# Kernel tuning notes

Hardware: AMD Instinct MI355X
Metric: run time of the kernel (lower is better)

## Reference

```python
import jax, jax.numpy as jnp
import numpy as np

ANCHORS = np.array([[10,13],[16,30],[33,23],[30,61],[62,45],[59,119],[116,90],[156,198],[373,326]], dtype=np.float32)
ANCHOR_MASK = [[6,7,8],[3,4,5],[0,1,2]]
CLASS_NUM = 80
IGNORE_THRESH = 0.5


def _bce_mean(z, x):
    # Keras BinaryCrossentropy(from_logits=True) called as a loss object:
    # elementwise sigmoid-CE, mean over last axis, then SUM_OVER_BATCH_SIZE
    # reduction == mean over ALL elements -> scalar.
    ce = jnp.maximum(x, 0.0) - x * z + jnp.log1p(jnp.exp(-jnp.abs(x)))
    return jnp.mean(ce)


def _layer_loss(out, lab, anchors):
    B, gh, gw, _ = out.shape
    A = anchors.shape[0]
    feats = out.reshape(B, gh, gw, A, CLASS_NUM + 5)
    anchors = jnp.asarray(anchors, dtype=jnp.float32)  # [A,2] (w,h)
    inp_wh = jnp.array([gw * 32, gh * 32], dtype=jnp.float32)  # reverse(input_shape)
    grid_wh = jnp.array([gw, gh], dtype=jnp.float32)           # reverse(grid_shape)

    gy, gx = jnp.meshgrid(jnp.arange(gh), jnp.arange(gw), indexing='ij')
    grid = jnp.stack([gx, gy], axis=-1).astype(jnp.float32)[:, :, None, :]  # [gh,gw,1,2]

    pred_xy = (jax.nn.sigmoid(feats[..., 0:2]) + grid) / grid_wh
    pred_wh = jnp.exp(feats[..., 2:4]) * anchors / inp_wh
    pred_box = jnp.concatenate([pred_xy, pred_wh], axis=-1)  # [B,gh,gw,A,4]

    obj = lab[..., 4:5]          # [B,gh,gw,A,1]
    objb = obj != 0.0
    N = gh * gw * A

    def _per_image(args):
        pb, tb, valid = args  # pb: [N,4] predicted, tb: [N,4] label boxes, valid: [N] bool
        b1_xy, b1_wh = pb[:, None, 0:2], pb[:, None, 2:4]
        b2_xy, b2_wh = tb[None, :, 0:2], tb[None, :, 2:4]
        b1_mins, b1_maxes = b1_xy - b1_wh / 2.0, b1_xy + b1_wh / 2.0
        b2_mins, b2_maxes = b2_xy - b2_wh / 2.0, b2_xy + b2_wh / 2.0
        inter_mins = jnp.maximum(b1_mins, b2_mins)
        inter_maxes = jnp.maximum(b1_maxes, b2_maxes)  # faithful to source (uses maximum, not minimum)
        inter_wh = jnp.maximum(inter_maxes - inter_mins, 0.0)
        inter = inter_wh[..., 0] * inter_wh[..., 1]
        a1 = b1_wh[..., 0] * b1_wh[..., 1]
        a2 = b2_wh[..., 0] * b2_wh[..., 1]
        iou = inter / (a1 + a2 - inter)  # [N,N]
        # only true boxes count; empty set -> best=-1 (matches tf reduce_max of empty = -inf)
        iou = jnp.where(valid[None, :], iou, -1.0)
        best_iou = jnp.max(iou, axis=-1)
        return (best_iou < IGNORE_THRESH).astype(jnp.float32)

    ignore = jax.lax.map(_per_image, (pred_box.reshape(B, N, 4),
                                      lab[..., 0:4].reshape(B, N, 4),
                                      objb.reshape(B, N)))
    ignore = jax.lax.stop_gradient(ignore).reshape(B, gh, gw, A, 1)

    raw_true_xy = lab[..., 0:2] * grid_wh - grid
    raw_true_wh = jnp.log(lab[..., 2:4] * inp_wh / anchors)
    raw_true_wh = jnp.where(objb, raw_true_wh, 0.0)
    box_loss_scale = 2.0 - lab[..., 2:3] * lab[..., 3:4]

    bf = jnp.float32(B)
    xy_loss = jnp.sum(obj * box_loss_scale * _bce_mean(raw_true_xy, feats[..., 0:2])) / bf
    wh_loss = jnp.sum(obj * box_loss_scale * 0.5 * jnp.square(raw_true_wh - feats[..., 2:4])) / bf
    conf_bce = _bce_mean(obj, feats[..., 4:5])
    conf_loss = jnp.sum(obj * conf_bce + (1.0 - obj) * conf_bce * ignore) / bf
    class_loss = jnp.sum(obj * _bce_mean(lab[..., 5:], feats[..., 5:])) / bf
    return xy_loss + wh_loss + conf_loss + class_loss


def _make_labels(key, B, g):
    k1, k2, k3, k4 = jax.random.split(key, 4)
    xy = jax.random.uniform(k1, (B, g, g, 3, 2), dtype=jnp.float32)
    wh = jax.random.uniform(k2, (B, g, g, 3, 2), dtype=jnp.float32, minval=0.05, maxval=1.0)
    objness = (jax.random.uniform(k3, (B, g, g, 3, 1)) < 0.02).astype(jnp.float32)
    cls = (jax.random.uniform(k4, (B, g, g, 3, CLASS_NUM)) < 0.05).astype(jnp.float32)
    return jnp.concatenate([xy, wh, objness, cls], axis=-1)


def setup_inputs() -> dict:
    key = jax.random.key(0)
    ks = jax.random.split(key, 6)
    B = 8
    grids = [13, 26, 52]
    out = {}
    for i, g in enumerate(grids):
        out[f'o{i}'] = jax.random.normal(ks[i], (B, g, g, 3 * (CLASS_NUM + 5)), dtype=jnp.float32)
        out[f'l{i}'] = _make_labels(ks[3 + i], B, g)
    return out


def reference(o0, o1, o2, l0, l1, l2):
    outputs = (o0, o1, o2)
    labels = (l0, l1, l2)
    loss = jnp.float32(0.0)
    for l in range(3):
        loss = loss + _layer_loss(outputs[l], labels[l], ANCHORS[ANCHOR_MASK[l]])
    return loss
```

## Files before the change

### kernel.cpp

```cpp
#include <hip/hip_runtime.h>
#include <math.h>

#define BDIM 256
#define NSTREAMB 1769
#define NCELLB 334
#define NBLK_A (NSTREAMB + NCELLB)

__device__ __constant__ float c_aw[3][3] = {{116.f,156.f,373.f},{30.f,62.f,59.f},{10.f,16.f,33.f}};
__device__ __constant__ float c_ah[3][3] = {{90.f,198.f,326.f},{61.f,45.f,119.f},{13.f,30.f,23.f}};


__device__ __forceinline__ float bce_fast(float z, float x) {
    float t = __expf(-fabsf(x));
    return fmaxf(x, 0.f) - x * z + __logf(1.f + t);
}
__device__ __forceinline__ float bce4(const float4& z, const float4& x) {
    return bce_fast(z.x, x.x) + bce_fast(z.y, x.y)
         + bce_fast(z.z, x.z) + bce_fast(z.w, x.w);
}

__global__ __launch_bounds__(BDIM) void mega_a(
    const float* __restrict__ o0, const float* __restrict__ l0,
    const float* __restrict__ o1, const float* __restrict__ l1,
    const float* __restrict__ o2, const float* __restrict__ l2,
    double* __restrict__ acc, int* __restrict__ cnt, float4* __restrict__ tbox,
    float4* __restrict__ pbox, float* __restrict__ noobj)
{
    if (blockIdx.x < NSTREAMB) {
        int layer, blk0, n4;
        const float4 *O4, *L4;
        if (blockIdx.x < 85)       { layer=0; blk0=0;   n4=86190;   O4=(const float4*)o0; L4=(const float4*)l0; }
        else if (blockIdx.x < 422) { layer=1; blk0=85;  n4=344760;  O4=(const float4*)o1; L4=(const float4*)l1; }
        else                       { layer=2; blk0=422; n4=1379040; O4=(const float4*)o2; L4=(const float4*)l2; }

        int rb   = (int)blockIdx.x - blk0;
        int base = rb * (BDIM * 4) + (int)threadIdx.x;
        float s0 = 0.f, s1 = 0.f, s2 = 0.f, s3 = 0.f;
        if ((rb + 1) * (BDIM * 4) <= n4) {
            float4 a0 = O4[base];          float4 b0 = L4[base];
            float4 a1 = O4[base +   BDIM]; float4 b1 = L4[base +   BDIM];
            float4 a2 = O4[base + 2*BDIM]; float4 b2 = L4[base + 2*BDIM];
            float4 a3 = O4[base + 3*BDIM]; float4 b3 = L4[base + 3*BDIM];
            s0 = bce4(b0, a0); s1 = bce4(b1, a1);
            s2 = bce4(b2, a2); s3 = bce4(b3, a3);
        } else {
            #pragma unroll
            for (int k = 0; k < 4; k++) {
                int j = base + k * BDIM;
                if (j < n4) { float4 a = O4[j], b = L4[j]; s0 += bce4(b, a); }
            }
        }
        float s = (s0 + s1) + (s2 + s3);
        __shared__ float sb[4];
        #pragma unroll
        for (int off = 32; off > 0; off >>= 1) s += __shfl_down(s, off, 64);
        if ((threadIdx.x & 63) == 0) sb[threadIdx.x >> 6] = s;
        __syncthreads();
        if (threadIdx.x == 0) {
            double t = (double)sb[0] + (double)sb[1] + (double)sb[2] + (double)sb[3];
            atomicAdd(&acc[layer * 8 + 0], t);
        }
        return;
    }

    int cb = blockIdx.x - NSTREAMB;
    int layer, blk0;
    if (cb < 16)      { layer = 0; blk0 = 0; }
    else if (cb < 80) { layer = 1; blk0 = 16; }
    else              { layer = 2; blk0 = 80; }
    const int g     = (layer == 0) ? 13 : (layer == 1) ? 26 : 52;
    const int Nlimg = g * g * 3;
    const int Cl    = 8 * Nlimg;
    const int cbase = (layer == 0) ? 0 : (layer == 1) ? 4056 : 20280;
    const float* O  = (layer == 0) ? o0 : (layer == 1) ? o1 : o2;
    const float* L  = (layer == 0) ? l0 : (layer == 1) ? l1 : l2;
    const float gf  = (float)g;
    const float inp = gf * 32.f;

    int cell = (cb - blk0) * BDIM + (int)threadIdx.x;
    float s_sub=0.f, s_xy=0.f, s_wh=0.f, s_conf=0.f, s_obj=0.f, s_s1=0.f;
    if (cell < Cl) {
        const float* op = O + (size_t)cell * 85;
        const float* lp = L + (size_t)cell * 85;
        float x0=op[0], x1=op[1], x2=op[2], x3=op[3], x4=op[4];
        float lx=lp[0], ly=lp[1], lw=lp[2], lh=lp[3], lobj=lp[4];
        int a  = cell % 3;
        int xi = (cell / 3) % g;
        int yi = (cell / (3 * g)) % g;
        int b  = cell / Nlimg;
        float aw = c_aw[layer][a], ah = c_ah[layer][a];

        float c4 = bce_fast(lobj, x4);
        s_sub  = bce_fast(lx,x0) + bce_fast(ly,x1)
               + bce_fast(lw,x2) + bce_fast(lh,x3) + c4;
        s_conf = c4;
        s_obj  = lobj;
        s_xy   = bce_fast(lx*gf - (float)xi, x0) + bce_fast(ly*gf - (float)yi, x1);

        float px = (1.f/(1.f+expf(-x0)) + (float)xi) / gf;
        float py = (1.f/(1.f+expf(-x1)) + (float)yi) / gf;
        float pw = expf(x2) * aw / inp;
        float ph = expf(x3) * ah / inp;
        pbox[cbase + cell]  = make_float4(px, py, pw, ph);
        noobj[cbase + cell] = 1.f - lobj;

        if (lobj != 0.f) {
            float bls = 2.f - lw * lh;
            s_s1 = lobj * bls;
            float dw = logf(lw * inp / aw) - x2;
            float dh = logf(lh * inp / ah) - x3;
            s_wh = lobj * bls * 0.5f * (dw * dw + dh * dh);
            int idx = atomicAdd(&cnt[layer * 8 + b], 1);
            tbox[cbase + b * Nlimg + idx] = make_float4(lx, ly, lw, lh);
        }
    }

    __shared__ float sb6[6][4];
    float v[6] = {s_sub, s_xy, s_wh, s_conf, s_obj, s_s1};
    #pragma unroll
    for (int q = 0; q < 6; q++) {
        float x = v[q];
        #pragma unroll
        for (int off = 32; off > 0; off >>= 1) x += __shfl_down(x, off, 64);
        if ((threadIdx.x & 63) == 0) sb6[q][threadIdx.x >> 6] = x;
    }
    __syncthreads();
    if (threadIdx.x < 6) {
        int q = threadIdx.x;
        double t = (double)sb6[q][0] + (double)sb6[q][1]
                 + (double)sb6[q][2] + (double)sb6[q][3];
        atomicAdd(&acc[layer * 8 + 1 + q], t);
    }
}

#define TCAP 512
#define NB_IGNORE 336
__global__ __launch_bounds__(BDIM) void ignore_fin(
    double* __restrict__ acc, const int* __restrict__ cnt,
    const float4* __restrict__ tbox, const float4* __restrict__ pbox,
    const float* __restrict__ noobj, int* __restrict__ done,
    float* __restrict__ out)
{
    int layer, img, chunk;
    if (blockIdx.x < 16)      { layer = 0; img = blockIdx.x >> 1; chunk = blockIdx.x & 1; }
    else if (blockIdx.x < 80) { int t = blockIdx.x - 16; layer = 1; img = t >> 3; chunk = t & 7; }
    else                      { int t = blockIdx.x - 80; layer = 2; img = t >> 5; chunk = t & 31; }
    const int g     = (layer == 0) ? 13 : (layer == 1) ? 26 : 52;
    const int Nlimg = g * g * 3;
    const int cbase = (layer == 0) ? 0 : (layer == 1) ? 4056 : 20280;

    int ci = chunk * BDIM + (int)threadIdx.x;
    bool live = (ci < Nlimg);
    int cell = cbase + img * Nlimg + (live ? ci : 0);

    float pminx=0, pmaxx=0, pminy=0, pmaxy=0, a1=0, nb=0;
    if (live) {
        float4 p = pbox[cell];
        pminx = p.x - p.z*0.5f; pmaxx = p.x + p.z*0.5f;
        pminy = p.y - p.w*0.5f; pmaxy = p.y + p.w*0.5f;
        a1 = p.z * p.w;
        nb = noobj[cell];
    }
    int n = cnt[layer * 8 + img];
    const float4* tp = tbox + cbase + img * Nlimg;

    __shared__ float4 sT[TCAP];
    float best = -1.f;
    bool donef = !live;
    for (int t0 = 0; t0 < n; t0 += TCAP) {
        int tn = min(TCAP, n - t0);
        __syncthreads();
        for (int i = threadIdx.x; i < tn; i += BDIM) sT[i] = tp[t0 + i];
        __syncthreads();
        if (!donef) {
            for (int j = 0; j < tn; j++) {
                float4 t = sT[j];
                float hw = t.z*0.5f, hh = t.w*0.5f;
                float imnx = fmaxf(pminx, t.x - hw);
                float imxx = fmaxf(pmaxx, t.x + hw);
                float imny = fmaxf(pminy, t.y - hh);
                float imxy = fmaxf(pmaxy, t.y + hh);
                float iw = fmaxf(imxx - imnx, 0.f);
                float ih = fmaxf(imxy - imny, 0.f);
                float inter = iw * ih;
                float iou = inter / (a1 + t.z*t.w - inter);
                best = fmaxf(best, iou);
                if (best >= 0.5f) { donef = true; break; }
            }
        }
    }
    float v = (live && best < 0.5f) ? nb : 0.f;

    __shared__ float sb[4];
    #pragma unroll
    for (int off = 32; off > 0; off >>= 1) v += __shfl_down(v, off, 64);
    if ((threadIdx.x & 63) == 0) sb[threadIdx.x >> 6] = v;
    __syncthreads();
    if (threadIdx.x == 0) {
        double t = (double)sb[0] + (double)sb[1] + (double)sb[2] + (double)sb[3];
        atomicAdd(&acc[layer * 8 + 7], t);
        __threadfence();
        int old = atomicAdd(done, 1);
        if (old == NB_IGNORE - 1) {
            __threadfence();
            double loss = 0.0;
            const int gs[3] = {13, 26, 52};
            for (int l = 0; l < 3; l++) {
                double C = 8.0 * gs[l] * gs[l] * 3.0;
                double q[8];
                #pragma unroll
                for (int k = 0; k < 8; k++)
                    q[k] = __hip_atomic_load(&acc[l*8+k], __ATOMIC_RELAXED,
                                             __HIP_MEMORY_SCOPE_AGENT);
                double cls = (q[0] - q[1]) / (C * 80.0);
                loss += ( (q[2]/(C*2.0))*q[6] + q[3]
                        + (q[4]/C)*(q[5]+q[7]) + cls*q[5] ) / 8.0;
            }
            out[0] = (float)loss;
        }
    }
}

extern "C" void kernel_launch(void* const* d_in, const int* in_sizes, int n_in,
                              void* d_out, int out_size, void* d_ws, size_t ws_size,
                              hipStream_t stream)
{
    const float* o0 = (const float*)d_in[0];
    const float* l0 = (const float*)d_in[1];
    const float* o1 = (const float*)d_in[2];
    const float* l1 = (const float*)d_in[3];
    const float* o2 = (const float*)d_in[4];
    const float* l2 = (const float*)d_in[5];

    double* acc   = (double*)d_ws;
    int*    cnt   = (int*)((char*)d_ws + 192);
    int*    done  = (int*)((char*)d_ws + 288);
    float4* tbox  = (float4*)((char*)d_ws + 512);
    float4* pbox  = (float4*)((char*)d_ws + 1363328);
    float*  noobj = (float*)((char*)d_ws + 2726144);

    hipMemsetAsync(d_ws, 0, 512, stream);
    mega_a<<<NBLK_A, BDIM, 0, stream>>>(o0, l0, o1, l1, o2, l2,
                                        acc, cnt, tbox, pbox, noobj);
    ignore_fin<<<NB_IGNORE, BDIM, 0, stream>>>(acc, cnt, tbox, pbox, noobj,
                                               done, (float*)d_out);
}
```

Measured before the change: 147.3 us.

## Replace global atomics with per-block slots and ballot compaction, drop memset

The first kernel stops issuing double atomics into shared accumulators and instead writes one partial sum per block into slot arrays. Label boxes are compacted within each block using a wavefront ballot and popcount, and stored with a per-block count, which replaces the per-image atomic counters. The ignore kernel now gathers the boxes for its image from the relevant block ranges, and the last block reduces all slots in parallel. Accumulators are zeroed inside the kernel, so the separate memset launch is gone. This removes atomic contention and one launch, at the cost of more gather and compaction work in the ignore kernel.

```diff
diff --git a/kernel.cpp b/kernel.cpp
--- a/kernel.cpp
+++ b/kernel.cpp
@@ -5,6 +5,8 @@
 #define NSTREAMB 1769
 #define NCELLB 334
 #define NBLK_A (NSTREAMB + NCELLB)
+#define NB_IGNORE 336
+#define TCAP 512
 
 __device__ __constant__ float c_aw[3][3] = {{116.f,156.f,373.f},{30.f,62.f,59.f},{10.f,16.f,33.f}};
 __device__ __constant__ float c_ah[3][3] = {{90.f,198.f,326.f},{61.f,45.f,119.f},{13.f,30.f,23.f}};
@@ -23,15 +25,21 @@
     const float* __restrict__ o0, const float* __restrict__ l0,
     const float* __restrict__ o1, const float* __restrict__ l1,
     const float* __restrict__ o2, const float* __restrict__ l2,
-    double* __restrict__ acc, int* __restrict__ cnt, float4* __restrict__ tbox,
-    float4* __restrict__ pbox, float* __restrict__ noobj)
+    double* __restrict__ accq7, int* __restrict__ done,
+    double* __restrict__ slotS, double* __restrict__ slotC,
+    int* __restrict__ countB, int* __restrict__ cidxB,
+    float4* __restrict__ tboxB, float4* __restrict__ pbox,
+    float* __restrict__ noobj)
 {
     if (blockIdx.x < NSTREAMB) {
-        int layer, blk0, n4;
+        if (blockIdx.x == 0 && threadIdx.x == 0) {
+            accq7[0] = 0.0; accq7[1] = 0.0; accq7[2] = 0.0; *done = 0;
+        }
+        int blk0, n4;
         const float4 *O4, *L4;
-        if (blockIdx.x < 85)       { layer=0; blk0=0;   n4=86190;   O4=(const float4*)o0; L4=(const float4*)l0; }
-        else if (blockIdx.x < 422) { layer=1; blk0=85;  n4=344760;  O4=(const float4*)o1; L4=(const float4*)l1; }
-        else                       { layer=2; blk0=422; n4=1379040; O4=(const float4*)o2; L4=(const float4*)l2; }
+        if (blockIdx.x < 85)       { blk0=0;   n4=86190;   O4=(const float4*)o0; L4=(const float4*)l0; }
+        else if (blockIdx.x < 422) { blk0=85;  n4=344760;  O4=(const float4*)o1; L4=(const float4*)l1; }
+        else                       { blk0=422; n4=1379040; O4=(const float4*)o2; L4=(const float4*)l2; }
 
         int rb   = (int)blockIdx.x - blk0;
         int base = rb * (BDIM * 4) + (int)threadIdx.x;
@@ -56,18 +64,17 @@
         for (int off = 32; off > 0; off >>= 1) s += __shfl_down(s, off, 64);
         if ((threadIdx.x & 63) == 0) sb[threadIdx.x >> 6] = s;
         __syncthreads();
-        if (threadIdx.x == 0) {
-            double t = (double)sb[0] + (double)sb[1] + (double)sb[2] + (double)sb[3];
-            atomicAdd(&acc[layer * 8 + 0], t);
-        }
+        if (threadIdx.x == 0)
+            slotS[blockIdx.x] = (double)sb[0] + (double)sb[1]
+                              + (double)sb[2] + (double)sb[3];
         return;
     }
 
     int cb = blockIdx.x - NSTREAMB;
-    int layer, blk0;
-    if (cb < 16)      { layer = 0; blk0 = 0; }
-    else if (cb < 80) { layer = 1; blk0 = 16; }
-    else              { layer = 2; blk0 = 80; }
+    int layer, cblk0;
+    if (cb < 16)      { layer = 0; cblk0 = 0; }
+    else if (cb < 80) { layer = 1; cblk0 = 16; }
+    else              { layer = 2; cblk0 = 80; }
     const int g     = (layer == 0) ? 13 : (layer == 1) ? 26 : 52;
     const int Nlimg = g * g * 3;
     const int Cl    = 8 * Nlimg;
@@ -77,9 +84,12 @@
     const float gf  = (float)g;
     const float inp = gf * 32.f;
 
-    int cell = (cb - blk0) * BDIM + (int)threadIdx.x;
+    int  cell = (cb - cblk0) * BDIM + (int)threadIdx.x;
+    bool live = (cell < Cl);
     float s_sub=0.f, s_xy=0.f, s_wh=0.f, s_conf=0.f, s_obj=0.f, s_s1=0.f;
-    if (cell < Cl) {
+    bool  f = false;
+    float tlx=0.f, tly=0.f, tlw=0.f, tlh=0.f;
+    if (live) {
         const float* op = O + (size_t)cell * 85;
         const float* lp = L + (size_t)cell * 85;
         float x0=op[0], x1=op[1], x2=op[2], x3=op[3], x4=op[4];
@@ -87,7 +97,6 @@
         int a  = cell % 3;
         int xi = (cell / 3) % g;
         int yi = (cell / (3 * g)) % g;
-        int b  = cell / Nlimg;
         float aw = c_aw[layer][a], ah = c_ah[layer][a];
 
         float c4 = bce_fast(lobj, x4);
@@ -110,10 +119,26 @@
             float dw = logf(lw * inp / aw) - x2;
             float dh = logf(lh * inp / ah) - x3;
             s_wh = lobj * bls * 0.5f * (dw * dw + dh * dh);
-            int idx = atomicAdd(&cnt[layer * 8 + b], 1);
-            tbox[cbase + b * Nlimg + idx] = make_float4(lx, ly, lw, lh);
-        }
-    }
+            f = true; tlx = lx; tly = ly; tlw = lw; tlh = lh;
+        }
+    }
+
+    unsigned long long m = __ballot(f);
+    int lane = threadIdx.x & 63, wid = threadIdx.x >> 6;
+    __shared__ int wcnt[4];
+    if (lane == 0) wcnt[wid] = __popcll(m);
+    int pos = __popcll(m & ((1ull << lane) - 1));
+    __syncthreads();
+    int wbase = 0;
+    #pragma unroll
+    for (int w = 0; w < 4; w++) if (w < wid) wbase += wcnt[w];
+    if (f) {
+        int p = cb * BDIM + wbase + pos;
+        tboxB[p] = make_float4(tlx, tly, tlw, tlh);
+        cidxB[p] = cell;
+    }
+    if (threadIdx.x == 0)
+        countB[cb] = wcnt[0] + wcnt[1] + wcnt[2] + wcnt[3];
 
     __shared__ float sb6[6][4];
     float v[6] = {s_sub, s_xy, s_wh, s_conf, s_obj, s_s1};
@@ -127,19 +152,17 @@
     __syncthreads();
     if (threadIdx.x < 6) {
         int q = threadIdx.x;
-        double t = (double)sb6[q][0] + (double)sb6[q][1]
-                 + (double)sb6[q][2] + (double)sb6[q][3];
-        atomicAdd(&acc[layer * 8 + 1 + q], t);
-    }
-}
-
-#define TCAP 512
-#define NB_IGNORE 336
+        slotC[cb * 6 + q] = (double)sb6[q][0] + (double)sb6[q][1]
+                          + (double)sb6[q][2] + (double)sb6[q][3];
+    }
+}
+
 __global__ __launch_bounds__(BDIM) void ignore_fin(
-    double* __restrict__ acc, const int* __restrict__ cnt,
-    const float4* __restrict__ tbox, const float4* __restrict__ pbox,
-    const float* __restrict__ noobj, int* __restrict__ done,
-    float* __restrict__ out)
+    double* __restrict__ accq7, int* __restrict__ done,
+    const double* __restrict__ slotS, const double* __restrict__ slotC,
+    const int* __restrict__ countB, const int* __restrict__ cidxB,
+    const float4* __restrict__ tboxB, const float4* __restrict__ pbox,
+    const float* __restrict__ noobj, float* __restrict__ out)
 {
     int layer, img, chunk;
     if (blockIdx.x < 16)      { layer = 0; img = blockIdx.x >> 1; chunk = blockIdx.x & 1; }
@@ -148,6 +171,7 @@
     const int g     = (layer == 0) ? 13 : (layer == 1) ? 26 : 52;
     const int Nlimg = g * g * 3;
     const int cbase = (layer == 0) ? 0 : (layer == 1) ? 4056 : 20280;
+    const int cblk0 = (layer == 0) ? 0 : (layer == 1) ? 16 : 80;
 
     int ci = chunk * BDIM + (int)threadIdx.x;
     bool live = (ci < Nlimg);
@@ -161,63 +185,135 @@
         a1 = p.z * p.w;
         nb = noobj[cell];
     }
-    int n = cnt[layer * 8 + img];
-    const float4* tp = tbox + cbase + img * Nlimg;
-
+
+    int b0 = cblk0 + (img * Nlimg) / BDIM;
+    int b1 = cblk0 + ((img + 1) * Nlimg - 1) / BDIM;
+    int nbk = b1 - b0 + 1;
+
+    __shared__ int    sCnt[40];
+    __shared__ int    sN;
     __shared__ float4 sT[TCAP];
+    for (int i = threadIdx.x; i < nbk; i += BDIM) sCnt[i] = countB[b0 + i];
+    if (threadIdx.x == 0) sN = 0;
+
     float best = -1.f;
     bool donef = !live;
-    for (int t0 = 0; t0 < n; t0 += TCAP) {
-        int tn = min(TCAP, n - t0);
+
+#define IOU_SCAN(TN)                                                         \
+    if (!donef) {                                                            \
+        for (int j = 0; j < (TN); j++) {                                     \
+            float4 t = sT[j];                                                \
+            float hw = t.z*0.5f, hh = t.w*0.5f;                              \
+                         \
+            float imnx = fmaxf(pminx, t.x - hw);                             \
+            float imxx = fmaxf(pmaxx, t.x + hw);                             \
+            float imny = fmaxf(pminy, t.y - hh);                             \
+            float imxy = fmaxf(pmaxy, t.y + hh);                             \
+            float iw = fmaxf(imxx - imnx, 0.f);                              \
+            float ih = fmaxf(imxy - imny, 0.f);                              \
+            float inter = iw * ih;                                           \
+            float iou = inter / (a1 + t.z*t.w - inter);                      \
+            best = fmaxf(best, iou);                                         \
+            if (best >= 0.5f) { donef = true; break; }                       \
+        }                                                                    \
+    }
+
+    for (int bi = 0; bi < nbk; ++bi) {
         __syncthreads();
-        for (int i = threadIdx.x; i < tn; i += BDIM) sT[i] = tp[t0 + i];
-        __syncthreads();
-        if (!donef) {
-            for (int j = 0; j < tn; j++) {
-                float4 t = sT[j];
-                float hw = t.z*0.5f, hh = t.w*0.5f;
-                float imnx = fmaxf(pminx, t.x - hw);
-                float imxx = fmaxf(pmaxx, t.x + hw);
-                float imny = fmaxf(pminy, t.y - hh);
-                float imxy = fmaxf(pmaxy, t.y + hh);
-                float iw = fmaxf(imxx - imnx, 0.f);
-                float ih = fmaxf(imxy - imny, 0.f);
-                float inter = iw * ih;
-                float iou = inter / (a1 + t.z*t.w - inter);
-                best = fmaxf(best, iou);
-                if (best >= 0.5f) { donef = true; break; }
+        int n = sCnt[bi];
+        if (sN + n > TCAP) {
+            int tn = sN;
+            IOU_SCAN(tn);
+            __syncthreads();
+            if (threadIdx.x == 0) sN = 0;
+            __syncthreads();
+        }
+        int gbase = (b0 + bi) * BDIM;
+        for (int i = threadIdx.x; i < n; i += BDIM) {
+            int cidx = cidxB[gbase + i];
+            if (cidx / Nlimg == img) {
+                int p = atomicAdd(&sN, 1);
+                sT[p] = tboxB[gbase + i];
             }
         }
     }
+    __syncthreads();
+    {
+        int tn = sN;
+        IOU_SCAN(tn);
+    }
+
     float v = (live && best < 0.5f) ? nb : 0.f;
-
-    __shared__ float sb[4];
+    __shared__ float sbr[4];
     #pragma unroll
     for (int off = 32; off > 0; off >>= 1) v += __shfl_down(v, off, 64);
-    if ((threadIdx.x & 63) == 0) sb[threadIdx.x >> 6] = v;
-    __syncthreads();
+    if ((threadIdx.x & 63) == 0) sbr[threadIdx.x >> 6] = v;
+    __syncthreads();
+    __shared__ int isLast;
     if (threadIdx.x == 0) {
-        double t = (double)sb[0] + (double)sb[1] + (double)sb[2] + (double)sb[3];
-        atomicAdd(&acc[layer * 8 + 7], t);
+        double t = (double)sbr[0] + (double)sbr[1] + (double)sbr[2] + (double)sbr[3];
+        atomicAdd(&accq7[layer], t);
         __threadfence();
         int old = atomicAdd(done, 1);
-        if (old == NB_IGNORE - 1) {
-            __threadfence();
-            double loss = 0.0;
-            const int gs[3] = {13, 26, 52};
-            for (int l = 0; l < 3; l++) {
-                double C = 8.0 * gs[l] * gs[l] * 3.0;
-                double q[8];
-                #pragma unroll
-                for (int k = 0; k < 8; k++)
-                    q[k] = __hip_atomic_load(&acc[l*8+k], __ATOMIC_RELAXED,
-                                             __HIP_MEMORY_SCOPE_AGENT);
-                double cls = (q[0] - q[1]) / (C * 80.0);
-                loss += ( (q[2]/(C*2.0))*q[6] + q[3]
-                        + (q[4]/C)*(q[5]+q[7]) + cls*q[5] ) / 8.0;
+        isLast = (old == NB_IGNORE - 1) ? 1 : 0;
+    }
+    __syncthreads();
+    if (!isLast) return;
+
+    __threadfence();
+    double qs0=0, qs1=0, qs2=0;
+    for (int i = threadIdx.x; i < NSTREAMB; i += BDIM) {
+        double x = slotS[i];
+        if (i < 85) qs0 += x; else if (i < 422) qs1 += x; else qs2 += x;
+    }
+    double c00=0,c01=0,c02=0,c03=0,c04=0,c05=0;
+    double c10=0,c11=0,c12=0,c13=0,c14=0,c15=0;
+    double c20=0,c21=0,c22=0,c23=0,c24=0,c25=0;
+#define CSUM(LO, HI, A0,A1,A2,A3,A4,A5)                                      \
+    for (int i = (LO)*6 + (int)threadIdx.x; i < (HI)*6; i += BDIM) {         \
+        int q = i % 6; double x = slotC[i];                                  \
+        if      (q == 0) A0 += x; else if (q == 1) A1 += x;                  \
+        else if (q == 2) A2 += x; else if (q == 3) A3 += x;                  \
+        else if (q == 4) A4 += x; else             A5 += x;                  \
+    }
+    CSUM(0,   16,  c00,c01,c02,c03,c04,c05)
+    CSUM(16,  80,  c10,c11,c12,c13,c14,c15)
+    CSUM(80,  334, c20,c21,c22,c23,c24,c25)
+
+    __shared__ double dsum[21][4];
+    {
+        double vals[21] = {qs0,qs1,qs2,
+                           c00,c01,c02,c03,c04,c05,
+                           c10,c11,c12,c13,c14,c15,
+                           c20,c21,c22,c23,c24,c25};
+        int lane = threadIdx.x & 63, wid = threadIdx.x >> 6;
+        #pragma unroll
+        for (int k = 0; k < 21; k++) {
+            double r = vals[k];
+            #pragma unroll
+            for (int off = 32; off > 0; off >>= 1) r += __shfl_down(r, off, 64);
+            if (lane == 0) dsum[k][wid] = r;
+        }
+    }
+    __syncthreads();
+    if (threadIdx.x == 0) {
+        double loss = 0.0;
+        const int gsz[3] = {13, 26, 52};
+        for (int l = 0; l < 3; l++) {
+            double C = 8.0 * gsz[l] * gsz[l] * 3.0;
+            double Q0 = dsum[l][0] + dsum[l][1] + dsum[l][2] + dsum[l][3];
+            double Qs[6];
+            for (int j = 0; j < 6; j++) {
+                int k = 3 + l * 6 + j;
+                Qs[j] = dsum[k][0] + dsum[k][1] + dsum[k][2] + dsum[k][3];
             }
-            out[0] = (float)loss;
-        }
+            double q7 = __hip_atomic_load(&accq7[l], __ATOMIC_RELAXED,
+                                          __HIP_MEMORY_SCOPE_AGENT);
+            double cls = (Q0 - Qs[0]) / (C * 80.0);
+            loss += ( (Qs[1]/(C*2.0))*Qs[5] + Qs[2]
+                    + (Qs[3]/C)*(Qs[4]+q7) + cls*Qs[4] ) / 8.0;
+        }
+        out[0] = (float)loss;
     }
 }
 
@@ -232,16 +328,20 @@
     const float* o2 = (const float*)d_in[4];
     const float* l2 = (const float*)d_in[5];
 
-    double* acc   = (double*)d_ws;
-    int*    cnt   = (int*)((char*)d_ws + 192);
-    int*    done  = (int*)((char*)d_ws + 288);
-    float4* tbox  = (float4*)((char*)d_ws + 512);
-    float4* pbox  = (float4*)((char*)d_ws + 1363328);
-    float*  noobj = (float*)((char*)d_ws + 2726144);
-
-    hipMemsetAsync(d_ws, 0, 512, stream);
+    double* accq7  = (double*)d_ws;
+    int*    done   = (int*)((char*)d_ws + 24);
+    double* slotS  = (double*)((char*)d_ws + 64);
+    double* slotC  = (double*)((char*)d_ws + 14336);
+    int*    countB = (int*)((char*)d_ws + 30720);
+    int*    cidxB  = (int*)((char*)d_ws + 32768);
+    float4* tboxB  = (float4*)((char*)d_ws + 375296);
+    float4* pbox   = (float4*)((char*)d_ws + 1742848);
+    float*  noobj  = (float*)((char*)d_ws + 3105664);
+
     mega_a<<<NBLK_A, BDIM, 0, stream>>>(o0, l0, o1, l1, o2, l2,
-                                        acc, cnt, tbox, pbox, noobj);
-    ignore_fin<<<NB_IGNORE, BDIM, 0, stream>>>(acc, cnt, tbox, pbox, noobj,
-                                               done, (float*)d_out);
-}
+                                        accq7, done, slotS, slotC,
+                                        countB, cidxB, tboxB, pbox, noobj);
+    ignore_fin<<<NB_IGNORE, BDIM, 0, stream>>>(accq7, done, slotS, slotC,
+                                               countB, cidxB, tboxB, pbox,
+                                               noobj, (float*)d_out);
+}
```

New measurement: 163.0 us. 10.6% more time.
